# Optimization experiments

Measured on AMD Instinct MI355X. Metric: run time of the kernel, lower is better.

The kernel has to match this reference:

```python
import jax, jax.numpy as jnp
import numpy as np

N_NODES = 50000
N_EDGES = 600000
D_IN = 128
D_OUT = 128
BN_EPS = 1e-5


def setup_inputs() -> dict:
    key = jax.random.key(0)
    k1, k2, k3, k4 = jax.random.split(key, 4)
    x = jax.random.normal(k1, (N_NODES, D_IN), dtype=jnp.float32)
    edge_index = jax.random.randint(k2, (2, N_EDGES), 0, N_NODES, dtype=jnp.int64)
    W = jax.random.normal(k3, (D_OUT, D_IN), dtype=jnp.float32) * (1.0 / np.sqrt(D_IN))
    b = jax.random.normal(k4, (D_OUT,), dtype=jnp.float32) * 0.01
    gamma = jnp.ones((D_OUT,), dtype=jnp.float32)
    beta = jnp.zeros((D_OUT,), dtype=jnp.float32)
    return {"x": x, "edge_index": edge_index, "W": W, "b": b, "gamma": gamma, "beta": beta}


def reference(x, edge_index, W, b, gamma, beta):
    n = x.shape[0]
    row, col = edge_index[0], edge_index[1]
    # degree of each destination node, clamped to >= 1
    deg = jnp.clip(jnp.bincount(row, length=n).astype(x.dtype), 1.0, None)
    # gather neighbor features and scatter-add by destination (row)
    agg = jax.ops.segment_sum(x[col], row, num_segments=n)  # [N, D_in]
    h = x + agg / deg[:, None]
    # linear: h @ W.T + b
    y = jnp.einsum('nd,od->no', h, W) + b  # [N, D_out]
    # BatchNorm1d (training mode: batch stats, biased variance)
    mean = jnp.mean(y, axis=0)
    var = jnp.mean((y - mean) ** 2, axis=0)
    y = (y - mean) * jax.lax.rsqrt(var + BN_EPS) * gamma + beta
    return jax.nn.relu(y)
```

## Files before the change

### kernel.cpp

```cpp
#include <hip/hip_runtime.h>

#define NN 50000
#define NE 600000
#define D 128
#define BN_EPS 1e-5f
#define NPART 8
#define KSEG 16

typedef __attribute__((ext_vector_type(8))) short bf16x8;
typedef __attribute__((ext_vector_type(4))) float f32x4;
typedef __attribute__((ext_vector_type(8))) unsigned int uintx8;
typedef unsigned int uint;
typedef unsigned short ushort;

__device__ __forceinline__ ushort f2bf(float f) {
    uint u = __float_as_uint(f);
    uint r = (u + 0x7fffu + ((u >> 16) & 1u)) >> 16;
    return (ushort)r;
}
__device__ __forceinline__ float bflo(uint v) { return __uint_as_float(v << 16); }
__device__ __forceinline__ float bfhi(uint v) { return __uint_as_float(v & 0xffff0000u); }

__global__ __launch_bounds__(256) void gemm_zw(const float* __restrict__ x,
                                               const float* __restrict__ W,
                                               ushort* __restrict__ zb,
                                               int* __restrict__ deg8,
                                               float* __restrict__ colsum,
                                               float* __restrict__ colsq) {
    __shared__ ushort Wl[D * D];
    int t = threadIdx.x;

    for (int i = blockIdx.x * 256 + t; i < NPART * NN; i += gridDim.x * 256)
        deg8[i] = 0;
    if (blockIdx.x == 0 && t < D) { colsum[t] = 0.f; colsq[t] = 0.f; }

    for (int i = t; i < D * D; i += 256) {
        int cc = i >> 7, k = i & 127;
        int g = (k >> 3) ^ (cc & 7);
        Wl[cc * 128 + g * 8 + (k & 7)] = f2bf(W[i]);
    }
    __syncthreads();

    int lane = t & 63;
    int wv = t >> 6;
    int row0 = blockIdx.x * 64 + wv * 16;
    int kb = lane >> 4;
    int ar = row0 + (lane & 15);
    if (ar >= NN) ar = NN - 1;

    const float* xr = x + (size_t)ar * D;
    bf16x8 afr[4];
    #pragma unroll
    for (int ks = 0; ks < 4; ks++) {
        int k0 = ks * 32 + kb * 8;
        float4 u = *(const float4*)(xr + k0);
        float4 v = *(const float4*)(xr + k0 + 4);
        bf16x8 f;
        f[0] = (short)f2bf(u.x); f[1] = (short)f2bf(u.y);
        f[2] = (short)f2bf(u.z); f[3] = (short)f2bf(u.w);
        f[4] = (short)f2bf(v.x); f[5] = (short)f2bf(v.y);
        f[6] = (short)f2bf(v.z); f[7] = (short)f2bf(v.w);
        afr[ks] = f;
    }

    int rbase = row0 + (lane >> 4) * 4;
    int cmask = (lane & 15) & 7;

    #pragma unroll
    for (int nt = 0; nt < 8; nt++) {
        int cc = nt * 16 + (lane & 15);
        const ushort* wr = Wl + cc * 128;
        bf16x8 b0 = *(const bf16x8*)(wr + (((0 * 4 + kb) ^ cmask) << 3));
        bf16x8 b1 = *(const bf16x8*)(wr + (((1 * 4 + kb) ^ cmask) << 3));
        bf16x8 b2 = *(const bf16x8*)(wr + (((2 * 4 + kb) ^ cmask) << 3));
        bf16x8 b3 = *(const bf16x8*)(wr + (((3 * 4 + kb) ^ cmask) << 3));

        f32x4 acc = {0.f, 0.f, 0.f, 0.f};
        acc = __builtin_amdgcn_mfma_f32_16x16x32_bf16(afr[0], b0, acc, 0, 0, 0);
        acc = __builtin_amdgcn_mfma_f32_16x16x32_bf16(afr[1], b1, acc, 0, 0, 0);
        acc = __builtin_amdgcn_mfma_f32_16x16x32_bf16(afr[2], b2, acc, 0, 0, 0);
        acc = __builtin_amdgcn_mfma_f32_16x16x32_bf16(afr[3], b3, acc, 0, 0, 0);

        #pragma unroll
        for (int r = 0; r < 4; r++) {
            int rr = rbase + r;
            if (rr < NN) zb[(size_t)rr * D + cc] = f2bf(acc[r]);
        }
    }
}

__global__ __launch_bounds__(256) void bucket_fill(const int* __restrict__ row,
                                                   const int* __restrict__ col,
                                                   int* __restrict__ deg8,
                                                   ushort* __restrict__ adj8) {
    int e = blockIdx.x * 256 + threadIdx.x;
    if (e < NE) {
        int p = blockIdx.x & (NPART - 1);
        int r = row[e];
        int c = col[e];
        int slot = atomicAdd(&deg8[p * NN + r], 1);
        if (slot < KSEG)
            adj8[(((size_t)(p * NN + r)) << 4) + slot] = (ushort)c;
    }
}

__global__ __launch_bounds__(256) void gather_z(const uint* __restrict__ zb,
                                                const int* __restrict__ deg8,
                                                const ushort* __restrict__ adj8,
                                                uint* __restrict__ yb) {
    int gw = (blockIdx.x * blockDim.x + threadIdx.x) >> 6;
    int lane = threadIdx.x & 63;
    if (gw >= NN) return;
    int qw = lane >> 4;
    int ql = lane & 15;

    int pA = qw, pB = qw + 4;
    int dA = deg8[pA * NN + gw];
    int dB = deg8[pB * NN + gw];
    int cA = (dA < KSEG) ? dA : KSEG;
    int cB = (dB < KSEG) ? dB : KSEG;
    uintx8 wA = *(const uintx8*)(adj8 + (((size_t)(pA * NN + gw)) << 4));
    uintx8 wB = *(const uintx8*)(adj8 + (((size_t)(pB * NN + gw)) << 4));

    uint4 xs = ((const uint4*)(zb + (size_t)gw * (D / 2)))[ql];

    float a[8] = {0.f, 0.f, 0.f, 0.f, 0.f, 0.f, 0.f, 0.f};
    #pragma unroll
    for (int j = 0; j < KSEG; j++) {
        if (j < cA) {
            int nb = (j & 1) ? (int)(wA[j >> 1] >> 16) : (int)(wA[j >> 1] & 0xffffu);
            uint4 v = ((const uint4*)(zb + (size_t)nb * (D / 2)))[ql];
            a[0] += bflo(v.x); a[1] += bfhi(v.x);
            a[2] += bflo(v.y); a[3] += bfhi(v.y);
            a[4] += bflo(v.z); a[5] += bfhi(v.z);
            a[6] += bflo(v.w); a[7] += bfhi(v.w);
        }
    }
    #pragma unroll
    for (int j = 0; j < KSEG; j++) {
        if (j < cB) {
            int nb = (j & 1) ? (int)(wB[j >> 1] >> 16) : (int)(wB[j >> 1] & 0xffffu);
            uint4 v = ((const uint4*)(zb + (size_t)nb * (D / 2)))[ql];
            a[0] += bflo(v.x); a[1] += bfhi(v.x);
            a[2] += bflo(v.y); a[3] += bfhi(v.y);
            a[4] += bflo(v.z); a[5] += bfhi(v.z);
            a[6] += bflo(v.w); a[7] += bfhi(v.w);
        }
    }

    int dsum = dA + dB;
    #pragma unroll
    for (int k = 0; k < 8; k++) {
        a[k] += __shfl_xor(a[k], 16);
        a[k] += __shfl_xor(a[k], 32);
    }
    dsum += __shfl_xor(dsum, 16);
    dsum += __shfl_xor(dsum, 32);

    if (qw == 0) {
        float inv = (dsum > 0) ? (1.0f / (float)dsum) : 0.f;
        uint4 o;
        o.x = (uint)f2bf(bflo(xs.x) + a[0] * inv) | ((uint)f2bf(bfhi(xs.x) + a[1] * inv) << 16);
        o.y = (uint)f2bf(bflo(xs.y) + a[2] * inv) | ((uint)f2bf(bfhi(xs.y) + a[3] * inv) << 16);
        o.z = (uint)f2bf(bflo(xs.z) + a[4] * inv) | ((uint)f2bf(bfhi(xs.z) + a[5] * inv) << 16);
        o.w = (uint)f2bf(bflo(xs.w) + a[6] * inv) | ((uint)f2bf(bfhi(xs.w) + a[7] * inv) << 16);
        ((uint4*)(yb + (size_t)gw * (D / 2)))[ql] = o;
    }
}

__global__ __launch_bounds__(256) void stats(const uint* __restrict__ yb,
                                             float* __restrict__ colsum,
                                             float* __restrict__ colsq) {
    __shared__ float lsum[D], lsq[D];
    int t = threadIdx.x;
    int lane = t & 63;
    if (t < D) { lsum[t] = 0.f; lsq[t] = 0.f; }
    __syncthreads();

    const int total = NN * D / 4;
    int gsz = gridDim.x * 256;
    int i0 = blockIdx.x * 256 + t;
    int c = (i0 * 4) & 127;
    float s0 = 0.f, s1 = 0.f, s2 = 0.f, s3 = 0.f;
    float q0 = 0.f, q1 = 0.f, q2 = 0.f, q3 = 0.f;
    for (int i = i0; i < total; i += gsz) {
        uint2 yv = ((const uint2*)yb)[i];
        float f0 = bflo(yv.x), f1 = bfhi(yv.x), f2 = bflo(yv.y), f3 = bfhi(yv.y);
        s0 += f0; q0 += f0 * f0;
        s1 += f1; q1 += f1 * f1;
        s2 += f2; q2 += f2 * f2;
        s3 += f3; q3 += f3 * f3;
    }
    s0 += __shfl_xor(s0, 32); q0 += __shfl_xor(q0, 32);
    s1 += __shfl_xor(s1, 32); q1 += __shfl_xor(q1, 32);
    s2 += __shfl_xor(s2, 32); q2 += __shfl_xor(q2, 32);
    s3 += __shfl_xor(s3, 32); q3 += __shfl_xor(q3, 32);
    if (lane < 32) {
        atomicAdd(&lsum[c],     s0); atomicAdd(&lsq[c],     q0);
        atomicAdd(&lsum[c + 1], s1); atomicAdd(&lsq[c + 1], q1);
        atomicAdd(&lsum[c + 2], s2); atomicAdd(&lsq[c + 2], q2);
        atomicAdd(&lsum[c + 3], s3); atomicAdd(&lsq[c + 3], q3);
    }
    __syncthreads();
    if (t < D) {
        atomicAdd(&colsum[t], lsum[t]);
        atomicAdd(&colsq[t], lsq[t]);
    }
}

__global__ __launch_bounds__(256) void bn_relu(const uint* __restrict__ yb,
                                               float* __restrict__ out,
                                               const float* __restrict__ colsum,
                                               const float* __restrict__ colsq,
                                               const float* __restrict__ gamma,
                                               const float* __restrict__ beta) {
    int i = blockIdx.x * blockDim.x + threadIdx.x;
    if (i >= NN * D / 4) return;
    uint2 yv = ((const uint2*)yb)[i];
    float yf[4] = {bflo(yv.x), bfhi(yv.x), bflo(yv.y), bfhi(yv.y)};
    int c = (i * 4) & 127;
    float4 v;
    float* vp = (float*)&v;
    #pragma unroll
    for (int j = 0; j < 4; j++) {
        float mean = colsum[c + j] * (1.0f / NN);
        float var  = colsq[c + j] * (1.0f / NN) - mean * mean;
        float sc = gamma[c + j] * rsqrtf(var + BN_EPS);
        float sh = beta[c + j] - mean * sc;
        vp[j] = fmaxf(0.f, yf[j] * sc + sh);
    }
    ((float4*)out)[i] = v;
}

extern "C" void kernel_launch(void* const* d_in, const int* in_sizes, int n_in,
                              void* d_out, int out_size, void* d_ws, size_t ws_size,
                              hipStream_t stream) {
    const float* x     = (const float*)d_in[0];
    const int*   edge  = (const int*)d_in[1];
    const float* W     = (const float*)d_in[2];
    const float* gamma = (const float*)d_in[4];
    const float* beta  = (const float*)d_in[5];
    float* out = (float*)d_out;

    const int* row = edge;
    const int* col = edge + NE;

    char* w = (char*)d_ws;
    auto alloc = [&](size_t bytes) {
        char* p = w;
        w += (bytes + 255) & ~(size_t)255;
        return p;
    };
    int*    deg8   = (int*)alloc((size_t)NPART * NN * 4);
    ushort* adj8   = (ushort*)alloc((size_t)NPART * NN * KSEG * 2);
    float*  colsum = (float*)alloc(D * 4);
    float*  colsq  = (float*)alloc(D * 4);
    uint*   zb     = (uint*)alloc((size_t)NN * (D / 2) * 4);
    uint*   yb     = (uint*)alloc((size_t)NN * (D / 2) * 4);

    gemm_zw<<<(NN + 63) / 64, 256, 0, stream>>>(x, W, (ushort*)zb, deg8, colsum, colsq);
    bucket_fill<<<(NE + 255) / 256, 256, 0, stream>>>(row, col, deg8, adj8);
    gather_z<<<(NN * 64 + 255) / 256, 256, 0, stream>>>(zb, deg8, adj8, yb);
    stats<<<512, 256, 0, stream>>>(yb, colsum, colsq);
    bn_relu<<<(NN * D / 4 + 255) / 256, 256, 0, stream>>>(yb, out, colsum, colsq, gamma, beta);
}
```

Measured before the change: 106.8 us.

## Fuse batchnorm column statistics into gather kernel with partitioned atomics

Removes the separate stats kernel and accumulates per-column sum and sum of squares inside gather_z via shared-memory atomics, then flushes to 8 partitioned global accumulators that bn_relu reduces. This avoids re-reading the bf16 intermediate and one kernel launch. It adds LDS atomic contention in the gather kernel and a small 8-way reduction per element in bn_relu.

```diff
diff --git a/kernel.cpp b/kernel.cpp
--- a/kernel.cpp
+++ b/kernel.cpp
@@ -25,14 +25,16 @@
                                                const float* __restrict__ W,
                                                ushort* __restrict__ zb,
                                                int* __restrict__ deg8,
-                                               float* __restrict__ colsum,
-                                               float* __restrict__ colsq) {
+                                               float* __restrict__ colsum8,
+                                               float* __restrict__ colsq8) {
     __shared__ ushort Wl[D * D];
     int t = threadIdx.x;
 
     for (int i = blockIdx.x * 256 + t; i < NPART * NN; i += gridDim.x * 256)
         deg8[i] = 0;
-    if (blockIdx.x == 0 && t < D) { colsum[t] = 0.f; colsq[t] = 0.f; }
+    if (blockIdx.x == 0) {
+        for (int i = t; i < NPART * D; i += 256) { colsum8[i] = 0.f; colsq8[i] = 0.f; }
+    }
 
     for (int i = t; i < D * D; i += 256) {
         int cc = i >> 7, k = i & 127;
@@ -107,10 +109,16 @@
 __global__ __launch_bounds__(256) void gather_z(const uint* __restrict__ zb,
                                                 const int* __restrict__ deg8,
                                                 const ushort* __restrict__ adj8,
-                                                uint* __restrict__ yb) {
-    int gw = (blockIdx.x * blockDim.x + threadIdx.x) >> 6;
-    int lane = threadIdx.x & 63;
-    if (gw >= NN) return;
+                                                uint* __restrict__ yb,
+                                                float* __restrict__ colsum8,
+                                                float* __restrict__ colsq8) {
+    __shared__ float lsum[D], lsq[D];
+    int t = threadIdx.x;
+    if (t < D) { lsum[t] = 0.f; lsq[t] = 0.f; }
+    __syncthreads();
+
+    int gw = (blockIdx.x * 256 + t) >> 6;
+    int lane = t & 63;
     int qw = lane >> 4;
     int ql = lane & 15;
 
@@ -159,59 +167,38 @@
 
     if (qw == 0) {
         float inv = (dsum > 0) ? (1.0f / (float)dsum) : 0.f;
+        float y0 = bflo(xs.x) + a[0] * inv, y1 = bfhi(xs.x) + a[1] * inv;
+        float y2 = bflo(xs.y) + a[2] * inv, y3 = bfhi(xs.y) + a[3] * inv;
+        float y4 = bflo(xs.z) + a[4] * inv, y5 = bfhi(xs.z) + a[5] * inv;
+        float y6 = bflo(xs.w) + a[6] * inv, y7 = bfhi(xs.w) + a[7] * inv;
         uint4 o;
-        o.x = (uint)f2bf(bflo(xs.x) + a[0] * inv) | ((uint)f2bf(bfhi(xs.x) + a[1] * inv) << 16);
-        o.y = (uint)f2bf(bflo(xs.y) + a[2] * inv) | ((uint)f2bf(bfhi(xs.y) + a[3] * inv) << 16);
-        o.z = (uint)f2bf(bflo(xs.z) + a[4] * inv) | ((uint)f2bf(bfhi(xs.z) + a[5] * inv) << 16);
-        o.w = (uint)f2bf(bflo(xs.w) + a[6] * inv) | ((uint)f2bf(bfhi(xs.w) + a[7] * inv) << 16);
+        o.x = (uint)f2bf(y0) | ((uint)f2bf(y1) << 16);
+        o.y = (uint)f2bf(y2) | ((uint)f2bf(y3) << 16);
+        o.z = (uint)f2bf(y4) | ((uint)f2bf(y5) << 16);
+        o.w = (uint)f2bf(y6) | ((uint)f2bf(y7) << 16);
         ((uint4*)(yb + (size_t)gw * (D / 2)))[ql] = o;
-    }
-}
-
-__global__ __launch_bounds__(256) void stats(const uint* __restrict__ yb,
-                                             float* __restrict__ colsum,
-                                             float* __restrict__ colsq) {
-    __shared__ float lsum[D], lsq[D];
-    int t = threadIdx.x;
-    int lane = t & 63;
-    if (t < D) { lsum[t] = 0.f; lsq[t] = 0.f; }
-    __syncthreads();
-
-    const int total = NN * D / 4;
-    int gsz = gridDim.x * 256;
-    int i0 = blockIdx.x * 256 + t;
-    int c = (i0 * 4) & 127;
-    float s0 = 0.f, s1 = 0.f, s2 = 0.f, s3 = 0.f;
-    float q0 = 0.f, q1 = 0.f, q2 = 0.f, q3 = 0.f;
-    for (int i = i0; i < total; i += gsz) {
-        uint2 yv = ((const uint2*)yb)[i];
-        float f0 = bflo(yv.x), f1 = bfhi(yv.x), f2 = bflo(yv.y), f3 = bfhi(yv.y);
-        s0 += f0; q0 += f0 * f0;
-        s1 += f1; q1 += f1 * f1;
-        s2 += f2; q2 += f2 * f2;
-        s3 += f3; q3 += f3 * f3;
-    }
-    s0 += __shfl_xor(s0, 32); q0 += __shfl_xor(q0, 32);
-    s1 += __shfl_xor(s1, 32); q1 += __shfl_xor(q1, 32);
-    s2 += __shfl_xor(s2, 32); q2 += __shfl_xor(q2, 32);
-    s3 += __shfl_xor(s3, 32); q3 += __shfl_xor(q3, 32);
-    if (lane < 32) {
-        atomicAdd(&lsum[c],     s0); atomicAdd(&lsq[c],     q0);
-        atomicAdd(&lsum[c + 1], s1); atomicAdd(&lsq[c + 1], q1);
-        atomicAdd(&lsum[c + 2], s2); atomicAdd(&lsq[c + 2], q2);
-        atomicAdd(&lsum[c + 3], s3); atomicAdd(&lsq[c + 3], q3);
+        int c0 = ql * 8;
+        atomicAdd(&lsum[c0 + 0], y0); atomicAdd(&lsq[c0 + 0], y0 * y0);
+        atomicAdd(&lsum[c0 + 1], y1); atomicAdd(&lsq[c0 + 1], y1 * y1);
+        atomicAdd(&lsum[c0 + 2], y2); atomicAdd(&lsq[c0 + 2], y2 * y2);
+        atomicAdd(&lsum[c0 + 3], y3); atomicAdd(&lsq[c0 + 3], y3 * y3);
+        atomicAdd(&lsum[c0 + 4], y4); atomicAdd(&lsq[c0 + 4], y4 * y4);
+        atomicAdd(&lsum[c0 + 5], y5); atomicAdd(&lsq[c0 + 5], y5 * y5);
+        atomicAdd(&lsum[c0 + 6], y6); atomicAdd(&lsq[c0 + 6], y6 * y6);
+        atomicAdd(&lsum[c0 + 7], y7); atomicAdd(&lsq[c0 + 7], y7 * y7);
     }
     __syncthreads();
     if (t < D) {
-        atomicAdd(&colsum[t], lsum[t]);
-        atomicAdd(&colsq[t], lsq[t]);
+        int p = blockIdx.x & (NPART - 1);
+        atomicAdd(&colsum8[p * D + t], lsum[t]);
+        atomicAdd(&colsq8[p * D + t], lsq[t]);
     }
 }
 
 __global__ __launch_bounds__(256) void bn_relu(const uint* __restrict__ yb,
                                                float* __restrict__ out,
-                                               const float* __restrict__ colsum,
-                                               const float* __restrict__ colsq,
+                                               const float* __restrict__ colsum8,
+                                               const float* __restrict__ colsq8,
                                                const float* __restrict__ gamma,
                                                const float* __restrict__ beta) {
     int i = blockIdx.x * blockDim.x + threadIdx.x;
@@ -223,8 +210,14 @@
     float* vp = (float*)&v;
     #pragma unroll
     for (int j = 0; j < 4; j++) {
-        float mean = colsum[c + j] * (1.0f / NN);
-        float var  = colsq[c + j] * (1.0f / NN) - mean * mean;
+        float cs = 0.f, cq = 0.f;
+        #pragma unroll
+        for (int p = 0; p < NPART; p++) {
+            cs += colsum8[p * D + c + j];
+            cq += colsq8[p * D + c + j];
+        }
+        float mean = cs * (1.0f / NN);
+        float var  = cq * (1.0f / NN) - mean * mean;
         float sc = gamma[c + j] * rsqrtf(var + BN_EPS);
         float sh = beta[c + j] - mean * sc;
         vp[j] = fmaxf(0.f, yf[j] * sc + sh);
@@ -251,16 +244,15 @@
         w += (bytes + 255) & ~(size_t)255;
         return p;
     };
-    int*    deg8   = (int*)alloc((size_t)NPART * NN * 4);
-    ushort* adj8   = (ushort*)alloc((size_t)NPART * NN * KSEG * 2);
-    float*  colsum = (float*)alloc(D * 4);
-    float*  colsq  = (float*)alloc(D * 4);
-    uint*   zb     = (uint*)alloc((size_t)NN * (D / 2) * 4);
-    uint*   yb     = (uint*)alloc((size_t)NN * (D / 2) * 4);
-
-    gemm_zw<<<(NN + 63) / 64, 256, 0, stream>>>(x, W, (ushort*)zb, deg8, colsum, colsq);
+    int*    deg8    = (int*)alloc((size_t)NPART * NN * 4);
+    ushort* adj8    = (ushort*)alloc((size_t)NPART * NN * KSEG * 2);
+    float*  colsum8 = (float*)alloc((size_t)NPART * D * 4);
+    float*  colsq8  = (float*)alloc((size_t)NPART * D * 4);
+    uint*   zb      = (uint*)alloc((size_t)NN * (D / 2) * 4);
+    uint*   yb      = (uint*)alloc((size_t)NN * (D / 2) * 4);
+
+    gemm_zw<<<(NN + 63) / 64, 256, 0, stream>>>(x, W, (ushort*)zb, deg8, colsum8, colsq8);
     bucket_fill<<<(NE + 255) / 256, 256, 0, stream>>>(row, col, deg8, adj8);
-    gather_z<<<(NN * 64 + 255) / 256, 256, 0, stream>>>(zb, deg8, adj8, yb);
-    stats<<<512, 256, 0, stream>>>(yb, colsum, colsq);
-    bn_relu<<<(NN * D / 4 + 255) / 256, 256, 0, stream>>>(yb, out, colsum, colsq, gamma, beta);
-}
+    gather_z<<<NN * 64 / 256, 256, 0, stream>>>(zb, deg8, adj8, yb, colsum8, colsq8);
+    bn_relu<<<(NN * D / 4 + 255) / 256, 256, 0, stream>>>(yb, out, colsum8, colsq8, gamma, beta);
+}
```

Result: slower. 150.9 us (+41.2%).
